# Kernel tuning notes

Measured on AMD Instinct MI355X. Metric: run time of the kernel, lower is better.

The kernel has to match this reference:

```python
import jax, jax.numpy as jnp
import numpy as np

B, T, D = 4, 4096, 2048
K = 1024
H, KVH, HD = 16, 4, 128
FF = 8192
EPS = 1e-6


def _rmsnorm(x, w):
    v = jnp.mean(x * x, axis=-1, keepdims=True)
    return x * jax.lax.rsqrt(v + EPS) * w


def _rotate_half(x):
    x1, x2 = jnp.split(x, 2, axis=-1)
    return jnp.concatenate([-x2, x1], axis=-1)


def setup_inputs() -> dict:
    key = jax.random.key(0)
    ks = jax.random.split(key, 16)
    hidden_states = jax.random.normal(ks[0], (B, T, D), dtype=jnp.float32)
    # unique sorted indices per sequence (top-k selection without duplicates)
    scores = jax.random.uniform(ks[1], (B, T))
    topk_indices = jnp.sort(jax.lax.top_k(scores, K)[1], axis=-1).astype(jnp.int64)
    gating_scores = jax.random.uniform(ks[2], (B, K), dtype=jnp.float32)
    # rotary embeddings over the full sequence [B, T, HD]
    inv = 1.0 / (10000.0 ** (jnp.arange(0, HD, 2, dtype=jnp.float32) / HD))
    ang = jnp.arange(T, dtype=jnp.float32)[:, None] * inv[None, :]  # [T, HD/2]
    emb = jnp.concatenate([ang, ang], axis=-1)
    cos = jnp.broadcast_to(jnp.cos(emb)[None], (B, T, HD)).astype(jnp.float32)
    sin = jnp.broadcast_to(jnp.sin(emb)[None], (B, T, HD)).astype(jnp.float32)
    s = 0.02
    params = dict(
        Wq=jax.random.normal(ks[3], (D, H * HD)) * s,
        bq=jnp.zeros((H * HD,)),
        Wk=jax.random.normal(ks[4], (D, KVH * HD)) * s,
        bk=jnp.zeros((KVH * HD,)),
        Wv=jax.random.normal(ks[5], (D, KVH * HD)) * s,
        bv=jnp.zeros((KVH * HD,)),
        Wo=jax.random.normal(ks[6], (H * HD, D)) * s,
        w_gate=jax.random.normal(ks[7], (D, FF)) * s,
        w_up=jax.random.normal(ks[8], (D, FF)) * s,
        w_down=jax.random.normal(ks[9], (FF, D)) * s,
        ln1_w=jnp.ones((D,)),
        ln2_w=jnp.ones((D,)),
    )
    return dict(hidden_states=hidden_states, topk_indices=topk_indices,
                gating_scores=gating_scores, cos=cos, sin=sin, **params)


def _decoder_layer(x, cos_s, sin_s, Wq, bq, Wk, bk, Wv, bv, Wo,
                   w_gate, w_up, w_down, ln1_w, ln2_w):
    # x: [B, K, D]; cos_s/sin_s: [B, K, HD]
    res = x
    h = _rmsnorm(x, ln1_w)
    q = (h @ Wq + bq).reshape(B, K, H, HD)
    k = (h @ Wk + bk).reshape(B, K, KVH, HD)
    v = (h @ Wv + bv).reshape(B, K, KVH, HD)
    c = cos_s[:, :, None, :]
    s = sin_s[:, :, None, :]
    q = q * c + _rotate_half(q) * s
    k = k * c + _rotate_half(k) * s
    # GQA: repeat kv heads
    k = jnp.repeat(k, H // KVH, axis=2)
    v = jnp.repeat(v, H // KVH, axis=2)
    scores = jnp.einsum('bqhd,bkhd->bhqk', q, k) / np.sqrt(HD)
    causal = jnp.tril(jnp.ones((K, K), dtype=bool))
    scores = jnp.where(causal[None, None], scores, jnp.finfo(scores.dtype).min)
    attn = jax.nn.softmax(scores, axis=-1)
    out = jnp.einsum('bhqk,bkhd->bqhd', attn, v).reshape(B, K, H * HD)
    x = res + out @ Wo
    # MLP (SwiGLU)
    res = x
    h = _rmsnorm(x, ln2_w)
    x = res + (jax.nn.silu(h @ w_gate) * (h @ w_up)) @ w_down
    return x


def reference(hidden_states, topk_indices, gating_scores, cos, sin,
              Wq, bq, Wk, bk, Wv, bv, Wo, w_gate, w_up, w_down, ln1_w, ln2_w):
    idx = topk_indices[:, :, None]  # [B, K, 1]
    selected = jnp.take_along_axis(hidden_states, idx, axis=1)  # [B, K, D]
    cos_s = jnp.take_along_axis(cos, idx, axis=1)
    sin_s = jnp.take_along_axis(sin, idx, axis=1)
    processed = _decoder_layer(selected, cos_s, sin_s, Wq, bq, Wk, bk, Wv, bv,
                               Wo, w_gate, w_up, w_down, ln1_w, ln2_w)
    # soft gating: selected + gate * (processed - selected)
    updated = selected + (processed - selected) * gating_scores[:, :, None]
    b_idx = jnp.arange(B)[:, None]
    final = hidden_states.at[b_idx, topk_indices].set(updated)
    return final
```

## Files before the change

### kernel.cpp

```cpp
#include <hip/hip_runtime.h>
#include <stdint.h>

typedef __bf16 bf16;
typedef __attribute__((ext_vector_type(8))) __bf16 bf16x8;
typedef __attribute__((ext_vector_type(4))) float f32x4;

namespace {

constexpr int cB = 4, cT = 4096, cD = 2048, cK = 1024, cH = 16, cKVH = 4, cHD = 128, cFF = 8192;
constexpr int cM = cB * cK;
constexpr int QKVW = cH * cHD + 2 * cKVH * cHD;

__device__ __forceinline__ void load_lds16(const void* g, void* l) {
  __builtin_amdgcn_global_load_lds((const __attribute__((address_space(1))) void*)g,
                                   (__attribute__((address_space(3))) void*)l, 16, 0, 0);
}

template <int N>
__device__ __forceinline__ void waitcnt_vm() {
  if constexpr (N == 0) asm volatile("s_waitcnt vmcnt(0)" ::: "memory");
  else if constexpr (N == 4) asm volatile("s_waitcnt vmcnt(4)" ::: "memory");
  else if constexpr (N == 6) asm volatile("s_waitcnt vmcnt(6)" ::: "memory");
  else if constexpr (N == 8) asm volatile("s_waitcnt vmcnt(8)" ::: "memory");
  else if constexpr (N == 9) asm volatile("s_waitcnt vmcnt(9)" ::: "memory");
  else if constexpr (N == 12) asm volatile("s_waitcnt vmcnt(12)" ::: "memory");
  else static_assert(N == 0, "unsupported vmcnt literal");
}

template <int OP>
__device__ __forceinline__ float blk_reduce(float v) {
  __shared__ float sm[5];
  const int tid = threadIdx.x, lane = tid & 63, wid = tid >> 6;
#pragma unroll
  for (int o = 32; o; o >>= 1) {
    float o2 = __shfl_down(v, o, 64);
    v = OP ? fmaxf(v, o2) : v + o2;
  }
  if (lane == 0) sm[wid] = v;
  __syncthreads();
  if (tid == 0) {
    float r = sm[0];
#pragma unroll
    for (int i = 1; i < 4; ++i) r = OP ? fmaxf(r, sm[i]) : r + sm[i];
    sm[4] = r;
  }
  __syncthreads();
  float r = sm[4];
  __syncthreads();
  return r;
}

template <int BN, int WM, int WN, int RING, class Epi>
__global__ __launch_bounds__(512, 2)
void gemm256(const bf16* __restrict__ A, int lda,
             const bf16* __restrict__ Bm, int ldb,
             int Kd, int GM, Epi epi) {
  constexpr int BM = 256;
  constexpr int FM = BM / WM / 16;
  constexpr int FN = BN / WN / 16;
  constexpr int ACALLS = 2;
  constexpr int BCALLS = BN / 128;
  constexpr int L = ACALLS + BCALLS;
  constexpr int D = RING - 1;
  constexpr int W = (D - 1) * L;
  constexpr int SLOTA = BM * 64;
  constexpr int SLOTB = BN * 64;
  constexpr int SLOT = SLOTA + SLOTB;
  __shared__ __align__(16) char lds[RING * SLOT];

  const int tid = threadIdx.x;
  const int lane = tid & 63;
  const int wid = tid >> 6;
  const int l15 = lane & 15, lq = lane >> 4;
  const int wr = wid / WN, wc = wid % WN;

  const int nwg = gridDim.x;
  const int xcd = blockIdx.x & 7, loc = blockIdx.x >> 3;
  const int wg = xcd * (nwg >> 3) + loc;
  const int GN = nwg / GM;
  const int per = 8 * GN;
  const int g = wg / per, r = wg % per;
  const int bm = g * 8 + (r & 7);
  const int bn = r >> 3;

  const bf16* Abase = A + (int64_t)bm * BM * lda;
  const bf16* Bbase = Bm + (int64_t)bn * BN * ldb;

  const bf16* srcA[ACALLS];
  int dstA[ACALLS];
#pragma unroll
  for (int c2 = 0; c2 < ACALLS; ++c2) {
    const int chunk = c2 * 512 + tid;
    const int row = chunk >> 2, pc = chunk & 3;
    const int lc = pc ^ ((row >> 1) & 3);
    srcA[c2] = Abase + (int64_t)row * lda + lc * 8;
    dstA[c2] = chunk * 16;
  }
  const bf16* srcB[BCALLS];
  int dstB[BCALLS];
#pragma unroll
  for (int c2 = 0; c2 < BCALLS; ++c2) {
    const int chunk = c2 * 512 + tid;
    const int row = chunk >> 2, pc = chunk & 3;
    const int lc = pc ^ ((row >> 1) & 3);
    srcB[c2] = Bbase + (int64_t)row * ldb + lc * 8;
    dstB[c2] = chunk * 16;
  }

  int offA[FM], offB[FN];
#pragma unroll
  for (int m = 0; m < FM; ++m) {
    const int row = wr * (BM / WM) + m * 16 + l15;
    offA[m] = row * 64 + (lq ^ ((row >> 1) & 3)) * 16;
  }
#pragma unroll
  for (int n = 0; n < FN; ++n) {
    const int row = wc * (BN / WN) + n * 16 + l15;
    offB[n] = SLOTA + row * 64 + (lq ^ ((row >> 1) & 3)) * 16;
  }

  const int KT = Kd >> 5;
  auto stage = [&](int t) {
    char* sb = lds + (size_t)(t % RING) * SLOT;
#pragma unroll
    for (int c2 = 0; c2 < ACALLS; ++c2)
      load_lds16(srcA[c2] + t * 32, sb + dstA[c2]);
#pragma unroll
    for (int c2 = 0; c2 < BCALLS; ++c2)
      load_lds16(srcB[c2] + t * 32, sb + SLOTA + dstB[c2]);
  };
  auto compute = [&](int t, f32x4 (&acc)[FM][FN]) {
    const char* sb = lds + (size_t)(t % RING) * SLOT;
    bf16x8 av[FM], bv[FN];
#pragma unroll
    for (int m = 0; m < FM; ++m) av[m] = *(const bf16x8*)(sb + offA[m]);
#pragma unroll
    for (int n = 0; n < FN; ++n) bv[n] = *(const bf16x8*)(sb + offB[n]);
    __builtin_amdgcn_s_setprio(1);
#pragma unroll
    for (int m = 0; m < FM; ++m)
#pragma unroll
      for (int n = 0; n < FN; ++n)
        acc[m][n] = __builtin_amdgcn_mfma_f32_16x16x32_bf16(av[m], bv[n], acc[m][n], 0, 0, 0);
    __builtin_amdgcn_s_setprio(0);
  };

  f32x4 acc[FM][FN] = {};

#pragma unroll
  for (int i = 0; i < D; ++i) stage(i);
  waitcnt_vm<W>();
  __builtin_amdgcn_s_barrier();
  __builtin_amdgcn_sched_barrier(0);

  for (int t = 0; t < KT - D; ++t) {
    stage(t + D);
    compute(t, acc);
    waitcnt_vm<W>();
    __builtin_amdgcn_s_barrier();
    __builtin_amdgcn_sched_barrier(0);
  }
  for (int t = KT - D; t < KT; ++t) {
    compute(t, acc);
    waitcnt_vm<0>();
    __builtin_amdgcn_s_barrier();
    __builtin_amdgcn_sched_barrier(0);
  }

#pragma unroll
  for (int m = 0; m < FM; ++m) {
    const int r0 = bm * BM + wr * (BM / WM) + m * 16 + lq * 4;
#pragma unroll
    for (int n = 0; n < FN; ++n) {
      const int c1 = bn * BN + wc * (BN / WN) + n * 16 + l15;
#pragma unroll
      for (int j = 0; j < 4; ++j) epi(r0 + j, c1, acc[m][n][j]);
    }
  }
}

struct EpiQKV {
  bf16* out; const float* bias;
  __device__ void operator()(int r, int c, float v) const {
    out[(int64_t)r * QKVW + c] = (bf16)(v + bias[c]);
  }
};
struct EpiOProj {
  float* x; const float* hidden; const int* topk;
  __device__ void operator()(int r, int c, float v) const {
    int b = r >> 10;
    int t = topk[r];
    x[(int64_t)r * cD + c] = v + hidden[((int64_t)b * cT + t) * cD + c];
  }
};
struct EpiBF16Out {
  bf16* out; int ldc;
  __device__ void operator()(int r, int c, float v) const {
    out[(int64_t)r * ldc + c] = (bf16)v;
  }
};
struct EpiUp {
  bf16* act;
  __device__ void operator()(int r, int c, float v) const {
    int64_t o = (int64_t)r * cFF + c;
    float g = (float)act[o];
    float s = g / (1.f + __expf(-g));
    act[o] = (bf16)(s * v);
  }
};
struct EpiDown {
  float* out; const float* x; const float* hidden; const int* topk; const float* gating;
  __device__ void operator()(int r, int c, float v) const {
    int b = r >> 10;
    int t = topk[r];
    float x2 = v + x[(int64_t)r * cD + c];
    int64_t ho = ((int64_t)b * cT + t) * cD + c;
    float sel = hidden[ho];
    out[ho] = sel + (x2 - sel) * gating[r];
  }
};

__global__ __launch_bounds__(256, 2) void flash_attn(const bf16* __restrict__ qkv,
                                                     const bf16* __restrict__ vt,
                                                     bf16* __restrict__ outb) {
  constexpr int QB = 64, KVB = 128;
  __shared__ __align__(16) char lds[81920];
  char* sK = lds;
  char* sP = lds + 32768;
  char* sV = lds + 49152;

  const int qt = blockIdx.x, h = blockIdx.y, b = blockIdx.z;
  const int kvh = h >> 2;
  const int qlo = qt * QB;
  const int tid = threadIdx.x, lane = tid & 63, wid = tid >> 6;
  const int l15 = lane & 15, lq = lane >> 4;
  const int wid16 = wid * 16;

  const bf16* qbase = qkv + (int64_t)(b * cK + qlo) * QKVW + h * cHD;
  const bf16* kbase = qkv + (int64_t)(b * cK) * QKVW + cH * cHD + kvh * cHD;
  const bf16* vtbase = vt + (int64_t)(b * cKVH + kvh) * cHD * cK;

#pragma unroll
  for (int c2 = 0; c2 < 4; ++c2) {
    int chunk = c2 * 256 + tid;
    int row = chunk >> 4, c16 = chunk & 15;
    load_lds16(qbase + (int64_t)row * QKVW + (c16 ^ (row & 15)) * 8, sK + chunk * 16);
  }
  __syncthreads();
  bf16x8 qf[4];
  {
    const int row = wid16 + l15;
#pragma unroll
    for (int kt = 0; kt < 4; ++kt)
      qf[kt] = *(const bf16x8*)(sK + row * 256 + (((kt * 4 + lq) ^ (row & 15)) * 16));
  }
  __syncthreads();

  f32x4 oacc[8] = {};
  float m_run[4], l_run[4];
#pragma unroll
  for (int j = 0; j < 4; ++j) { m_run[j] = -3.0e38f; l_run[j] = 0.f; }

  const int jmax = (qlo + QB - 1) >> 7;
  const float sl2e = 0.08838834764831845f * 1.44269504088896f;

  for (int jj = 0; jj <= jmax; ++jj) {
#pragma unroll
    for (int c2 = 0; c2 < 8; ++c2) {
      int chunk = c2 * 256 + tid;
      int row = chunk >> 4, c16 = chunk & 15;
      int cs = (c16 ^ (row & 15)) * 8;
      load_lds16(kbase + (int64_t)(jj * KVB + row) * QKVW + cs, sK + chunk * 16);
      load_lds16(vtbase + (int64_t)row * cK + jj * KVB + cs, sV + chunk * 16);
    }
    __syncthreads();

    f32x4 sacc[8] = {};
#pragma unroll
    for (int kt = 0; kt < 4; ++kt) {
      bf16x8 bv[8];
#pragma unroll
      for (int n = 0; n < 8; ++n) {
        int rk = n * 16 + l15;
        bv[n] = *(const bf16x8*)(sK + rk * 256 + (((kt * 4 + lq) ^ (rk & 15)) * 16));
      }
#pragma unroll
      for (int n = 0; n < 8; ++n)
        sacc[n] = __builtin_amdgcn_mfma_f32_16x16x32_bf16(qf[kt], bv[n], sacc[n], 0, 0, 0);
    }

    if (jj == jmax) {
#pragma unroll
      for (int n = 0; n < 8; ++n)
#pragma unroll
        for (int j = 0; j < 4; ++j) {
          int qrow = qlo + wid16 + lq * 4 + j;
          int kcol = jj * KVB + n * 16 + l15;
          if (kcol > qrow) sacc[n][j] = -3.0e38f;
        }
    }

#pragma unroll
    for (int j = 0; j < 4; ++j) {
      float mx = sacc[0][j];
#pragma unroll
      for (int n = 1; n < 8; ++n) mx = fmaxf(mx, sacc[n][j]);
#pragma unroll
      for (int off = 1; off < 16; off <<= 1) mx = fmaxf(mx, __shfl_xor(mx, off, 64));
      float mnew = fmaxf(m_run[j], mx);
      float corr = exp2f((m_run[j] - mnew) * sl2e);
      m_run[j] = mnew;
      float ps = 0.f;
#pragma unroll
      for (int n = 0; n < 8; ++n) {
        float p = exp2f((sacc[n][j] - mnew) * sl2e);
        sacc[n][j] = p;
        ps += p;
      }
#pragma unroll
      for (int off = 1; off < 16; off <<= 1) ps += __shfl_xor(ps, off, 64);
      l_run[j] = l_run[j] * corr + ps;
#pragma unroll
      for (int n = 0; n < 8; ++n) oacc[n][j] *= corr;
    }

#pragma unroll
    for (int n = 0; n < 8; ++n)
#pragma unroll
      for (int j = 0; j < 4; ++j) {
        int row = wid16 + lq * 4 + j;
        int col = n * 16 + l15;
        int c16 = (col >> 3) ^ (row & 15);
        *(bf16*)(sP + row * 256 + c16 * 16 + (col & 7) * 2) = (bf16)sacc[n][j];
      }
    __syncthreads();

#pragma unroll
    for (int kt = 0; kt < 4; ++kt) {
      const int prow = wid16 + l15;
      bf16x8 av = *(const bf16x8*)(sP + prow * 256 + (((kt * 4 + lq) ^ (prow & 15)) * 16));
      bf16x8 bv[8];
#pragma unroll
      for (int n = 0; n < 8; ++n) {
        int rd = n * 16 + l15;
        bv[n] = *(const bf16x8*)(sV + rd * 256 + (((kt * 4 + lq) ^ (rd & 15)) * 16));
      }
#pragma unroll
      for (int n = 0; n < 8; ++n)
        oacc[n] = __builtin_amdgcn_mfma_f32_16x16x32_bf16(av, bv[n], oacc[n], 0, 0, 0);
    }
    __syncthreads();
  }

#pragma unroll
  for (int j = 0; j < 4; ++j) {
    int row = qlo + wid16 + lq * 4 + j;
    float inv = 1.f / l_run[j];
#pragma unroll
    for (int n = 0; n < 8; ++n) {
      int col = h * cHD + n * 16 + l15;
      outb[((int64_t)b * cK + row) * cD + col] = (bf16)(oacc[n][j] * inv);
    }
  }
}

__global__ void copy_f4(const float4* __restrict__ s, float4* __restrict__ d, int64_t n) {
  int64_t i = (int64_t)blockIdx.x * blockDim.x + threadIdx.x;
  const int64_t st = (int64_t)gridDim.x * blockDim.x;
  for (; i < n; i += st) d[i] = s[i];
}

__global__ void wconv(const float* __restrict__ src, bf16* __restrict__ dst,
                      int R, int C, int coff, int ldd) {
  __shared__ float t[32][33];
  const int c0 = blockIdx.x * 32, r0 = blockIdx.y * 32;
  for (int rr = threadIdx.y; rr < 32; rr += 8)
    t[rr][threadIdx.x] = src[(int64_t)(r0 + rr) * C + c0 + threadIdx.x];
  __syncthreads();
  for (int rr = threadIdx.y; rr < 32; rr += 8)
    dst[(int64_t)(c0 + rr + coff) * ldd + r0 + threadIdx.x] = (bf16)t[threadIdx.x][rr];
}

__global__ void biascat(const float* __restrict__ bq, const float* __restrict__ bk,
                        const float* __restrict__ bv, float* __restrict__ o) {
  int i = blockIdx.x * 256 + threadIdx.x;
  if (i < QKVW) o[i] = (i < 2048) ? bq[i] : (i < 2560 ? bk[i - 2048] : bv[i - 2560]);
}

__global__ void rmsnorm_rows(const float* __restrict__ base, const int* __restrict__ topk,
                             const float* __restrict__ w, bf16* __restrict__ out) {
  const int r = blockIdx.x;
  const float* src;
  if (topk) {
    int t = topk[r];
    src = base + ((int64_t)(r >> 10) * cT + t) * cD;
  } else {
    src = base + (int64_t)r * cD;
  }
  const int tid = threadIdx.x;
  const float4* s4 = (const float4*)src;
  float4 a = s4[tid * 2], b = s4[tid * 2 + 1];
  float ss = a.x * a.x + a.y * a.y + a.z * a.z + a.w * a.w +
             b.x * b.x + b.y * b.y + b.z * b.z + b.w * b.w;
  float tot = blk_reduce<0>(ss);
  float sc = rsqrtf(tot * (1.f / cD) + 1e-6f);
  bf16* o = out + (int64_t)r * cD;
  const int d0 = tid * 8;
  o[d0 + 0] = (bf16)(a.x * sc * w[d0 + 0]);
  o[d0 + 1] = (bf16)(a.y * sc * w[d0 + 1]);
  o[d0 + 2] = (bf16)(a.z * sc * w[d0 + 2]);
  o[d0 + 3] = (bf16)(a.w * sc * w[d0 + 3]);
  o[d0 + 4] = (bf16)(b.x * sc * w[d0 + 4]);
  o[d0 + 5] = (bf16)(b.y * sc * w[d0 + 5]);
  o[d0 + 6] = (bf16)(b.z * sc * w[d0 + 6]);
  o[d0 + 7] = (bf16)(b.w * sc * w[d0 + 7]);
}

__global__ void rope_kernel(bf16* __restrict__ qkv, const float* __restrict__ cosb,
                            const float* __restrict__ sinb, const int* __restrict__ topk) {
  const int r = blockIdx.x;
  const int b = r >> 10;
  const int t = topk[r];
  const float* cr = cosb + ((int64_t)b * cT + t) * cHD;
  const float* sr = sinb + ((int64_t)b * cT + t) * cHD;
  bf16* rowq = qkv + (int64_t)r * QKVW;
  for (int p = threadIdx.x; p < (cH + cKVH) * 64; p += 256) {
    int hh = p >> 6, d = p & 63;
    bf16* base = (hh < cH) ? (rowq + hh * cHD) : (rowq + cH * cHD + (hh - cH) * cHD);
    float x1 = (float)base[d], x2 = (float)base[d + 64];
    float c1 = cr[d], s1 = sr[d], c2 = cr[d + 64], s2 = sr[d + 64];
    base[d] = (bf16)(x1 * c1 - x2 * s1);
    base[d + 64] = (bf16)(x2 * c2 + x1 * s2);
  }
}

__global__ void vtrans(const bf16* __restrict__ qkv, bf16* __restrict__ Vt) {
  __shared__ bf16 t[32][33];
  const int bz = blockIdx.z, b = bz >> 2, kv = bz & 3;
  const int k0 = blockIdx.x * 32, d0 = blockIdx.y * 32;
  for (int rr = threadIdx.y; rr < 32; rr += 8)
    t[rr][threadIdx.x] =
        qkv[(int64_t)(b * cK + k0 + rr) * QKVW + cH * cHD + cKVH * cHD + kv * cHD + d0 + threadIdx.x];
  __syncthreads();
  for (int rr = threadIdx.y; rr < 32; rr += 8)
    Vt[((int64_t)(b * cKVH + kv) * cHD + d0 + rr) * cK + k0 + threadIdx.x] = t[threadIdx.x][rr];
}

}

extern "C" void kernel_launch(void* const* d_in, const int* in_sizes, int n_in,
                              void* d_out, int out_size, void* d_ws, size_t ws_size,
                              hipStream_t stream) {
  const float* hidden = (const float*)d_in[0];
  const int* topk = (const int*)d_in[1];
  const float* gating = (const float*)d_in[2];
  const float* cosb = (const float*)d_in[3];
  const float* sinb = (const float*)d_in[4];
  const float* Wq = (const float*)d_in[5];
  const float* bq = (const float*)d_in[6];
  const float* Wk = (const float*)d_in[7];
  const float* bk = (const float*)d_in[8];
  const float* Wv = (const float*)d_in[9];
  const float* bv = (const float*)d_in[10];
  const float* Wo = (const float*)d_in[11];
  const float* wg = (const float*)d_in[12];
  const float* wu = (const float*)d_in[13];
  const float* wd = (const float*)d_in[14];
  const float* ln1 = (const float*)d_in[15];
  const float* ln2 = (const float*)d_in[16];
  float* out = (float*)d_out;
  (void)in_sizes; (void)n_in; (void)out_size; (void)ws_size;

  char* ws = (char*)d_ws;
  size_t off = 0;
  auto alloc = [&](size_t bytes) {
    char* p = ws + off;
    off += (bytes + 255) & ~(size_t)255;
    return p;
  };
  bf16* wt_qkv = (bf16*)alloc((size_t)QKVW * cD * 2);
  bf16* wt_o = (bf16*)alloc((size_t)cD * cD * 2);
  bf16* wt_g = (bf16*)alloc((size_t)cFF * cD * 2);
  bf16* wt_u = (bf16*)alloc((size_t)cFF * cD * 2);
  bf16* wt_d = (bf16*)alloc((size_t)cD * cFF * 2);
  float* bias_cat = (float*)alloc((size_t)QKVW * 4);
  bf16* hbuf = (bf16*)alloc((size_t)cM * cD * 2);
  bf16* qkv = (bf16*)alloc((size_t)cM * QKVW * 2);
  bf16* vt = (bf16*)alloc((size_t)cB * cKVH * cHD * cK * 2);
  bf16* attnout = (bf16*)alloc((size_t)cM * cD * 2);
  float* xbuf = (float*)alloc((size_t)cM * cD * 4);
  bf16* actbuf = (bf16*)alloc((size_t)cM * cFF * 2);

  copy_f4<<<2048, 256, 0, stream>>>((const float4*)hidden, (float4*)out,
                                    (int64_t)cB * cT * cD / 4);

  const dim3 tb(32, 8);
  wconv<<<dim3(cD / 32, cD / 32), tb, 0, stream>>>(Wq, wt_qkv, cD, cD, 0, cD);
  wconv<<<dim3(512 / 32, cD / 32), tb, 0, stream>>>(Wk, wt_qkv, cD, 512, 2048, cD);
  wconv<<<dim3(512 / 32, cD / 32), tb, 0, stream>>>(Wv, wt_qkv, cD, 512, 2560, cD);
  wconv<<<dim3(cD / 32, cD / 32), tb, 0, stream>>>(Wo, wt_o, cD, cD, 0, cD);
  wconv<<<dim3(cFF / 32, cD / 32), tb, 0, stream>>>(wg, wt_g, cD, cFF, 0, cD);
  wconv<<<dim3(cFF / 32, cD / 32), tb, 0, stream>>>(wu, wt_u, cD, cFF, 0, cD);
  wconv<<<dim3(cD / 32, cFF / 32), tb, 0, stream>>>(wd, wt_d, cFF, cD, 0, cFF);
  biascat<<<(QKVW + 255) / 256, 256, 0, stream>>>(bq, bk, bv, bias_cat);

  rmsnorm_rows<<<cM, 256, 0, stream>>>(hidden, topk, ln1, hbuf);
  gemm256<256, 2, 4, 4, EpiQKV><<<16 * (QKVW / 256), 512, 0, stream>>>(
      hbuf, cD, wt_qkv, cD, cD, 16, EpiQKV{qkv, bias_cat});
  rope_kernel<<<cM, 256, 0, stream>>>(qkv, cosb, sinb, topk);
  vtrans<<<dim3(cK / 32, cHD / 32, cB * cKVH), tb, 0, stream>>>(qkv, vt);

  flash_attn<<<dim3(cK / 64, cH, cB), 256, 0, stream>>>(qkv, vt, attnout);

  gemm256<128, 4, 2, 5, EpiOProj><<<16 * (cD / 128), 512, 0, stream>>>(
      attnout, cD, wt_o, cD, cD, 16, EpiOProj{xbuf, hidden, topk});
  rmsnorm_rows<<<cM, 256, 0, stream>>>(xbuf, nullptr, ln2, hbuf);
  gemm256<256, 2, 4, 4, EpiBF16Out><<<16 * (cFF / 256), 512, 0, stream>>>(
      hbuf, cD, wt_g, cD, cD, 16, EpiBF16Out{actbuf, cFF});
  gemm256<256, 2, 4, 4, EpiUp><<<16 * (cFF / 256), 512, 0, stream>>>(
      hbuf, cD, wt_u, cD, cD, 16, EpiUp{actbuf});
  gemm256<128, 4, 2, 5, EpiDown><<<16 * (cD / 128), 512, 0, stream>>>(
      actbuf, cFF, wt_d, cFF, cFF, 16, EpiDown{out, xbuf, hidden, topk, gating});
}
```

Baseline: 897.4 us.

## Fuse gate and up GEMMs with SwiGLU epilogue; pair-step pipeline for RING=5

Replaces the separate gate and up projection GEMMs with a single kernel that loads the A tile once, computes both gate and up accumulators, and applies SiLU(gate)*up in registers. This removes the bf16 round trip of the gate output through global memory and halves the A-tile traffic for the MLP input. The RING=5 GEMMs (O-proj and down) now stage and compute two K-steps per barrier, which cuts barrier count. The tail handling also changes to drain all loads before the last computes. The fused kernel doubles the accumulator registers, which may hurt occupancy or cause spills.

```diff
diff --git a/kernel.cpp b/kernel.cpp
--- a/kernel.cpp
+++ b/kernel.cpp
@@ -19,6 +19,7 @@
 template <int N>
 __device__ __forceinline__ void waitcnt_vm() {
   if constexpr (N == 0) asm volatile("s_waitcnt vmcnt(0)" ::: "memory");
+  else if constexpr (N == 3) asm volatile("s_waitcnt vmcnt(3)" ::: "memory");
   else if constexpr (N == 4) asm volatile("s_waitcnt vmcnt(4)" ::: "memory");
   else if constexpr (N == 6) asm volatile("s_waitcnt vmcnt(6)" ::: "memory");
   else if constexpr (N == 8) asm volatile("s_waitcnt vmcnt(8)" ::: "memory");
@@ -50,7 +51,7 @@
   return r;
 }
 
-template <int BN, int WM, int WN, int RING, class Epi>
+template <int BN, int WM, int WN, int RING, int UNROLL, class Epi>
 __global__ __launch_bounds__(512, 2)
 void gemm256(const bf16* __restrict__ A, int lda,
              const bf16* __restrict__ Bm, int ldb,
@@ -62,7 +63,6 @@
   constexpr int BCALLS = BN / 128;
   constexpr int L = ACALLS + BCALLS;
   constexpr int D = RING - 1;
-  constexpr int W = (D - 1) * L;
   constexpr int SLOTA = BM * 64;
   constexpr int SLOTB = BN * 64;
   constexpr int SLOT = SLOTA + SLOTB;
@@ -147,34 +147,176 @@
 
   f32x4 acc[FM][FN] = {};
 
+  if constexpr (UNROLL == 1) {
+#pragma unroll
+    for (int i = 0; i < D; ++i) stage(i);
+    waitcnt_vm<(D - 1) * L>();
+    __builtin_amdgcn_s_barrier();
+    __builtin_amdgcn_sched_barrier(0);
+    for (int t = 0; t < KT - D; ++t) {
+      stage(t + D);
+      compute(t, acc);
+      waitcnt_vm<(D - 1) * L>();
+      __builtin_amdgcn_s_barrier();
+      __builtin_amdgcn_sched_barrier(0);
+    }
+    waitcnt_vm<0>();
+    __builtin_amdgcn_s_barrier();
+    for (int t = KT - D; t < KT; ++t) compute(t, acc);
+  } else {
+    static_assert(RING == 5 && UNROLL == 2, "pair mode is RING=5");
+#pragma unroll
+    for (int i = 0; i < 3; ++i) stage(i);
+    waitcnt_vm<L>();
+    __builtin_amdgcn_s_barrier();
+    __builtin_amdgcn_sched_barrier(0);
+    int t = 0;
+    for (; t <= KT - 6; t += 2) {
+      stage(t + 3);
+      stage(t + 4);
+      compute(t, acc);
+      compute(t + 1, acc);
+      waitcnt_vm<L>();
+      __builtin_amdgcn_s_barrier();
+      __builtin_amdgcn_sched_barrier(0);
+    }
+    stage(KT - 1);
+    waitcnt_vm<0>();
+    __builtin_amdgcn_s_barrier();
+    compute(KT - 4, acc);
+    compute(KT - 3, acc);
+    compute(KT - 2, acc);
+    compute(KT - 1, acc);
+  }
+
+#pragma unroll
+  for (int m = 0; m < FM; ++m) {
+    const int r0 = bm * BM + wr * (BM / WM) + m * 16 + lq * 4;
+#pragma unroll
+    for (int n = 0; n < FN; ++n) {
+      const int c1 = bn * BN + wc * (BN / WN) + n * 16 + l15;
+#pragma unroll
+      for (int j = 0; j < 4; ++j) epi(r0 + j, c1, acc[m][n][j]);
+    }
+  }
+}
+
+__global__ __launch_bounds__(512, 2)
+void gemm_gateup(const bf16* __restrict__ A, const bf16* __restrict__ Bg,
+                 const bf16* __restrict__ Bu, bf16* __restrict__ act) {
+  constexpr int BM = 256, BN = 128, WM = 4, WN = 2;
+  constexpr int FM = 4, FN = 4;
+  constexpr int RING = 4, D = 3, L = 4;
+  constexpr int SLOTA = BM * 64, SLOTB = BN * 64;
+  constexpr int SLOT = SLOTA + 2 * SLOTB;
+  __shared__ __align__(16) char lds[RING * SLOT];
+
+  const int tid = threadIdx.x;
+  const int lane = tid & 63;
+  const int wid = tid >> 6;
+  const int l15 = lane & 15, lq = lane >> 4;
+  const int wr = wid / WN, wc = wid % WN;
+
+  const int nwg = gridDim.x;
+  const int xcd = blockIdx.x & 7, loc = blockIdx.x >> 3;
+  const int wg = xcd * (nwg >> 3) + loc;
+  const int GM = 16, GN = nwg / GM;
+  const int per = 8 * GN;
+  const int g = wg / per, r = wg % per;
+  const int bm = g * 8 + (r & 7);
+  const int bn = r >> 3;
+
+  const bf16* Abase = A + (int64_t)bm * BM * cD;
+  const bf16* Gbase = Bg + (int64_t)bn * BN * cD;
+  const bf16* Ubase = Bu + (int64_t)bn * BN * cD;
+
+  const bf16* srcA[2];
+  int dstA[2];
+#pragma unroll
+  for (int c2 = 0; c2 < 2; ++c2) {
+    const int chunk = c2 * 512 + tid;
+    const int row = chunk >> 2, pc = chunk & 3;
+    const int lc = pc ^ ((row >> 1) & 3);
+    srcA[c2] = Abase + (int64_t)row * cD + lc * 8;
+    dstA[c2] = chunk * 16;
+  }
+  const int brow = tid >> 2, bpc = tid & 3;
+  const int blc = bpc ^ ((brow >> 1) & 3);
+  const bf16* srcG = Gbase + (int64_t)brow * cD + blc * 8;
+  const bf16* srcU = Ubase + (int64_t)brow * cD + blc * 8;
+  const int dstBo = tid * 16;
+
+  int offA[FM], offB[FN];
+#pragma unroll
+  for (int m = 0; m < FM; ++m) {
+    const int row = wr * 64 + m * 16 + l15;
+    offA[m] = row * 64 + (lq ^ ((row >> 1) & 3)) * 16;
+  }
+#pragma unroll
+  for (int n = 0; n < FN; ++n) {
+    const int row = wc * 64 + n * 16 + l15;
+    offB[n] = row * 64 + (lq ^ ((row >> 1) & 3)) * 16;
+  }
+
+  const int KT = cD >> 5;
+  auto stage = [&](int t) {
+    char* sb = lds + (size_t)(t % RING) * SLOT;
+#pragma unroll
+    for (int c2 = 0; c2 < 2; ++c2) load_lds16(srcA[c2] + t * 32, sb + dstA[c2]);
+    load_lds16(srcG + t * 32, sb + SLOTA + dstBo);
+    load_lds16(srcU + t * 32, sb + SLOTA + SLOTB + dstBo);
+  };
+
+  f32x4 accg[FM][FN] = {}, accu[FM][FN] = {};
+
+  auto compute = [&](int t) {
+    const char* sb = lds + (size_t)(t % RING) * SLOT;
+    bf16x8 av[FM], gv[FN], uv[FN];
+#pragma unroll
+    for (int m = 0; m < FM; ++m) av[m] = *(const bf16x8*)(sb + offA[m]);
+#pragma unroll
+    for (int n = 0; n < FN; ++n) gv[n] = *(const bf16x8*)(sb + SLOTA + offB[n]);
+#pragma unroll
+    for (int n = 0; n < FN; ++n) uv[n] = *(const bf16x8*)(sb + SLOTA + SLOTB + offB[n]);
+    __builtin_amdgcn_s_setprio(1);
+#pragma unroll
+    for (int m = 0; m < FM; ++m)
+#pragma unroll
+      for (int n = 0; n < FN; ++n) {
+        accg[m][n] = __builtin_amdgcn_mfma_f32_16x16x32_bf16(av[m], gv[n], accg[m][n], 0, 0, 0);
+        accu[m][n] = __builtin_amdgcn_mfma_f32_16x16x32_bf16(av[m], uv[n], accu[m][n], 0, 0, 0);
+      }
+    __builtin_amdgcn_s_setprio(0);
+  };
+
 #pragma unroll
   for (int i = 0; i < D; ++i) stage(i);
-  waitcnt_vm<W>();
+  waitcnt_vm<(D - 1) * L>();
   __builtin_amdgcn_s_barrier();
   __builtin_amdgcn_sched_barrier(0);
-
   for (int t = 0; t < KT - D; ++t) {
     stage(t + D);
-    compute(t, acc);
-    waitcnt_vm<W>();
+    compute(t);
+    waitcnt_vm<(D - 1) * L>();
     __builtin_amdgcn_s_barrier();
     __builtin_amdgcn_sched_barrier(0);
   }
-  for (int t = KT - D; t < KT; ++t) {
-    compute(t, acc);
-    waitcnt_vm<0>();
-    __builtin_amdgcn_s_barrier();
-    __builtin_amdgcn_sched_barrier(0);
-  }
+  waitcnt_vm<0>();
+  __builtin_amdgcn_s_barrier();
+  for (int t = KT - D; t < KT; ++t) compute(t);
 
 #pragma unroll
   for (int m = 0; m < FM; ++m) {
-    const int r0 = bm * BM + wr * (BM / WM) + m * 16 + lq * 4;
+    const int r0 = bm * BM + wr * 64 + m * 16 + lq * 4;
 #pragma unroll
     for (int n = 0; n < FN; ++n) {
-      const int c1 = bn * BN + wc * (BN / WN) + n * 16 + l15;
-#pragma unroll
-      for (int j = 0; j < 4; ++j) epi(r0 + j, c1, acc[m][n][j]);
+      const int c1 = bn * BN + wc * 64 + n * 16 + l15;
+#pragma unroll
+      for (int j = 0; j < 4; ++j) {
+        float gvv = accg[m][n][j];
+        float s = gvv / (1.f + __expf(-gvv));
+        act[(int64_t)(r0 + j) * cFF + c1] = (bf16)(s * accu[m][n][j]);
+      }
     }
   }
 }
@@ -191,21 +333,6 @@
     int b = r >> 10;
     int t = topk[r];
     x[(int64_t)r * cD + c] = v + hidden[((int64_t)b * cT + t) * cD + c];
-  }
-};
-struct EpiBF16Out {
-  bf16* out; int ldc;
-  __device__ void operator()(int r, int c, float v) const {
-    out[(int64_t)r * ldc + c] = (bf16)v;
-  }
-};
-struct EpiUp {
-  bf16* act;
-  __device__ void operator()(int r, int c, float v) const {
-    int64_t o = (int64_t)r * cFF + c;
-    float g = (float)act[o];
-    float s = g / (1.f + __expf(-g));
-    act[o] = (bf16)(s * v);
   }
 };
 struct EpiDown {
@@ -505,20 +632,17 @@
   biascat<<<(QKVW + 255) / 256, 256, 0, stream>>>(bq, bk, bv, bias_cat);
 
   rmsnorm_rows<<<cM, 256, 0, stream>>>(hidden, topk, ln1, hbuf);
-  gemm256<256, 2, 4, 4, EpiQKV><<<16 * (QKVW / 256), 512, 0, stream>>>(
+  gemm256<256, 2, 4, 4, 1, EpiQKV><<<16 * (QKVW / 256), 512, 0, stream>>>(
       hbuf, cD, wt_qkv, cD, cD, 16, EpiQKV{qkv, bias_cat});
   rope_kernel<<<cM, 256, 0, stream>>>(qkv, cosb, sinb, topk);
   vtrans<<<dim3(cK / 32, cHD / 32, cB * cKVH), tb, 0, stream>>>(qkv, vt);
 
   flash_attn<<<dim3(cK / 64, cH, cB), 256, 0, stream>>>(qkv, vt, attnout);
 
-  gemm256<128, 4, 2, 5, EpiOProj><<<16 * (cD / 128), 512, 0, stream>>>(
+  gemm256<128, 4, 2, 5, 2, EpiOProj><<<16 * (cD / 128), 512, 0, stream>>>(
       attnout, cD, wt_o, cD, cD, 16, EpiOProj{xbuf, hidden, topk});
   rmsnorm_rows<<<cM, 256, 0, stream>>>(xbuf, nullptr, ln2, hbuf);
-  gemm256<256, 2, 4, 4, EpiBF16Out><<<16 * (cFF / 256), 512, 0, stream>>>(
-      hbuf, cD, wt_g, cD, cD, 16, EpiBF16Out{actbuf, cFF});
-  gemm256<256, 2, 4, 4, EpiUp><<<16 * (cFF / 256), 512, 0, stream>>>(
-      hbuf, cD, wt_u, cD, cD, 16, EpiUp{actbuf});
-  gemm256<128, 4, 2, 5, EpiDown><<<16 * (cD / 128), 512, 0, stream>>>(
+  gemm_gateup<<<16 * (cFF / 128), 512, 0, stream>>>(hbuf, wt_g, wt_u, actbuf);
+  gemm256<128, 4, 2, 5, 2, EpiDown><<<16 * (cD / 128), 512, 0, stream>>>(
       actbuf, cFF, wt_d, cFF, cFF, 16, EpiDown{out, xbuf, hidden, topk, gating});
 }
```

Result: faster. 868.2 us (-3.3%).
